# Kernel optimization log

Measured on AMD Instinct MI355X. Metric: run time of the kernel, lower is better.

## Reference

```python
import jax, jax.numpy as jnp
import numpy as np

B, N, S, H = 8, 512, 4096, 1024

def setup_inputs() -> dict:
    key = jax.random.key(0)
    k1, k2, k3 = jax.random.split(key, 3)
    doc_state = jax.random.normal(k1, (B, S, H), dtype=jnp.float32)
    # token->node membership mask (soft weights in [0,1), structurally a sparse/binary mask)
    nodes_mapping = jax.random.uniform(k2, (B, N, S), dtype=jnp.float32)
    # node lengths: positive, in [1, S) to avoid divide-by-near-zero
    nodes_len = jax.random.uniform(k3, (B, N), dtype=jnp.float32, minval=1.0, maxval=float(S))
    return {"doc_state": doc_state, "nodes_mapping": nodes_mapping, "nodes_len": nodes_len}

def reference(doc_state, nodes_mapping, nodes_len):
    # Faithful math: sum_s nodes_mapping[b,n,s] * doc_state[b,s,h] / nodes_len[b,n]
    # Expressed as a batched matmul instead of materializing [B,N,S,H].
    pooled = jnp.einsum('bns,bsh->bnh', nodes_mapping, doc_state)
    return pooled / nodes_len[:, :, None]
```

## Files before the change

kernel.cpp:

```cpp
#include <hip/hip_runtime.h>
#include <hip/hip_bf16.h>


typedef __bf16 bf16x8 __attribute__((ext_vector_type(8)));
typedef float  f32x4  __attribute__((ext_vector_type(4)));

#define MFMA16(a, b, c) __builtin_amdgcn_mfma_f32_16x16x32_bf16(a, b, c, 0, 0, 0)

constexpr int Bsz = 8;
constexpr int Nn  = 512;
constexpr int Ss  = 4096;
constexpr int Hh  = 1024;

constexpr int BM = 64, BN = 64, BK = 32;
constexpr int LDK = BK + 8;
constexpr int NT = Ss / BK;
constexpr int NWG = Bsz * (Nn / BM) * (Hh / BN);

__global__ __launch_bounds__(256, 4)
void mean_pool_gemm(const float* __restrict__ doc,
                    const float* __restrict__ map,
                    const float* __restrict__ len,
                    float* __restrict__ out)
{
    __shared__ __align__(16) __bf16 As[2][BM * LDK];
    __shared__ __align__(16) __bf16 Bs[2][BN * LDK];

    const int blk = (blockIdx.x & 7) * (NWG / 8) + (blockIdx.x >> 3);

    const int b   = blk >> 7;
    const int rem = blk & 127;
    const int mt  = rem >> 4;
    const int ht  = rem & 15;
    const int n0  = mt * BM;
    const int h0  = ht * BN;

    const int tid  = threadIdx.x;
    const int wave = tid >> 6;
    const int lane = tid & 63;
    const int wr   = wave >> 1;
    const int wc   = wave & 1;
    const int l15  = lane & 15;
    const int l4   = lane >> 4;

    const float* Ab = map + (size_t)b * Nn * Ss + (size_t)n0 * Ss;
    const float* Bb = doc + (size_t)b * Ss * Hh + h0;

    const int ra = tid >> 2;
    const int ka = (tid & 3) * 8;
    const int hbb = tid & 63;
    const int kb  = tid >> 6;

    f32x4 aR[2];
    float bR[8];
    f32x4 acc[2][2] = {};

    {
        const float* ap = Ab + (size_t)ra * Ss + ka;
        aR[0] = *(const f32x4*)(ap);
        aR[1] = *(const f32x4*)(ap + 4);
        const float* bp = Bb + (size_t)(kb * 8) * Hh + hbb;
        #pragma unroll
        for (int j = 0; j < 8; j++) bR[j] = bp[(size_t)j * Hh];

        bf16x8 va, vb;
        #pragma unroll
        for (int i = 0; i < 8; i++) {
            va[i] = (__bf16)aR[i >> 2][i & 3];
            vb[i] = (__bf16)bR[i];
        }
        *(bf16x8*)&As[0][ra * LDK + ka]      = va;
        *(bf16x8*)&Bs[0][hbb * LDK + kb * 8] = vb;
    }
    __syncthreads();

    int cur = 0;
    for (int t = 0; t < NT; ++t) {
        if (t + 1 < NT) {
            const int s0 = (t + 1) * BK;
            const float* ap = Ab + (size_t)ra * Ss + s0 + ka;
            aR[0] = *(const f32x4*)(ap);
            aR[1] = *(const f32x4*)(ap + 4);
            const float* bp = Bb + (size_t)(s0 + kb * 8) * Hh + hbb;
            #pragma unroll
            for (int j = 0; j < 8; j++) bR[j] = bp[(size_t)j * Hh];
        }

        {
            bf16x8 aF[2], bF[2];
            #pragma unroll
            for (int m = 0; m < 2; m++)
                aF[m] = *(const bf16x8*)&As[cur][(wr * 32 + m * 16 + l15) * LDK + l4 * 8];
            #pragma unroll
            for (int n = 0; n < 2; n++)
                bF[n] = *(const bf16x8*)&Bs[cur][(wc * 32 + n * 16 + l15) * LDK + l4 * 8];
            #pragma unroll
            for (int m = 0; m < 2; m++)
                #pragma unroll
                for (int n = 0; n < 2; n++)
                    acc[m][n] = MFMA16(aF[m], bF[n], acc[m][n]);
        }

        if (t + 1 < NT) {
            __syncthreads();
            bf16x8 va, vb;
            #pragma unroll
            for (int i = 0; i < 8; i++) {
                va[i] = (__bf16)aR[i >> 2][i & 3];
                vb[i] = (__bf16)bR[i];
            }
            *(bf16x8*)&As[cur ^ 1][ra * LDK + ka]      = va;
            *(bf16x8*)&Bs[cur ^ 1][hbb * LDK + kb * 8] = vb;
            __syncthreads();
            cur ^= 1;
        }
    }

    const float* lenb = len + b * Nn + n0 + wr * 32;
    float* ob = out + (size_t)b * Nn * Hh + (size_t)(n0 + wr * 32) * Hh + h0 + wc * 32;
    #pragma unroll
    for (int m = 0; m < 2; m++) {
        float inv[4];
        #pragma unroll
        for (int j = 0; j < 4; j++) inv[j] = 1.0f / lenb[m * 16 + l4 * 4 + j];
        #pragma unroll
        for (int n = 0; n < 2; n++) {
            #pragma unroll
            for (int j = 0; j < 4; j++) {
                const int row = m * 16 + l4 * 4 + j;
                ob[(size_t)row * Hh + n * 16 + l15] = acc[m][n][j] * inv[j];
            }
        }
    }
}

extern "C" void kernel_launch(void* const* d_in, const int* in_sizes, int n_in,
                              void* d_out, int out_size, void* d_ws, size_t ws_size,
                              hipStream_t stream) {
    const float* doc = (const float*)d_in[0];
    const float* map = (const float*)d_in[1];
    const float* len = (const float*)d_in[2];
    float* out = (float*)d_out;

    dim3 grid(NWG);
    dim3 block(256);
    hipLaunchKernelGGL(mean_pool_gemm, grid, block, 0, stream, doc, map, len, out);
}
```

Baseline: 316.9 us.

## Enlarge M tile and pipeline loads with one barrier per K step

Doubles the M tile to 128 rows, so each workgroup computes a 4x2 grid of MFMA fragments per wave. This halves how many workgroups re-read each doc_state tile. The K loop is unrolled by two, with two register stage sets and two LDS buffers. Each step issues global loads two tiles ahead, converts and stores the previous stage to LDS, computes on the current buffer, and then hits a single barrier instead of two. The cost is more registers, with launch bounds dropping to 2 blocks per CU, and a grid of only 512 workgroups.

```diff
diff --git a/kernel.cpp b/kernel.cpp
--- a/kernel.cpp
+++ b/kernel.cpp
@@ -12,24 +12,68 @@
 constexpr int Ss  = 4096;
 constexpr int Hh  = 1024;
 
-constexpr int BM = 64, BN = 64, BK = 32;
-constexpr int LDK = BK + 8;
-constexpr int NT = Ss / BK;
+constexpr int BM = 128, BN = 64, BK = 32;
+constexpr int LDK = 40;
+constexpr int NT  = Ss / BK;
 constexpr int NWG = Bsz * (Nn / BM) * (Hh / BN);
 
-__global__ __launch_bounds__(256, 4)
+struct StageRegs {
+    f32x4 a[4];
+    float b[8];
+};
+
+__device__ __forceinline__ void issue_loads(StageRegs& r, const float* Ab, const float* Bb,
+                                            int s0, int ra, int ka, int hbb, int kb) {
+    const float* ap = Ab + (size_t)ra * Ss + s0 + ka;
+    #pragma unroll
+    for (int i = 0; i < 4; i++) r.a[i] = *(const f32x4*)(ap + i * 4);
+    const float* bp = Bb + (size_t)(s0 + kb * 8) * Hh + hbb;
+    #pragma unroll
+    for (int j = 0; j < 8; j++) r.b[j] = bp[(size_t)j * Hh];
+}
+
+__device__ __forceinline__ void write_lds(__bf16* As, __bf16* Bs, const StageRegs& r,
+                                          int ra, int ka, int hbb, int kb) {
+    bf16x8 v0, v1, w;
+    #pragma unroll
+    for (int i = 0; i < 8; i++) {
+        v0[i] = (__bf16)r.a[i >> 2][i & 3];
+        v1[i] = (__bf16)r.a[2 + (i >> 2)][i & 3];
+        w[i]  = (__bf16)r.b[i];
+    }
+    *(bf16x8*)&As[ra * LDK + ka]     = v0;
+    *(bf16x8*)&As[ra * LDK + ka + 8] = v1;
+    *(bf16x8*)&Bs[hbb * LDK + kb * 8] = w;
+}
+
+__device__ __forceinline__ void compute(const __bf16* As, const __bf16* Bs,
+                                        f32x4 acc[4][2], int wr, int wc, int l15, int l4) {
+    bf16x8 aF[4], bF[2];
+    #pragma unroll
+    for (int m = 0; m < 4; m++)
+        aF[m] = *(const bf16x8*)&As[(wr * 64 + m * 16 + l15) * LDK + l4 * 8];
+    #pragma unroll
+    for (int n = 0; n < 2; n++)
+        bF[n] = *(const bf16x8*)&Bs[(wc * 32 + n * 16 + l15) * LDK + l4 * 8];
+    #pragma unroll
+    for (int m = 0; m < 4; m++)
+        #pragma unroll
+        for (int n = 0; n < 2; n++)
+            acc[m][n] = MFMA16(aF[m], bF[n], acc[m][n]);
+}
+
+__global__ __launch_bounds__(256, 2)
 void mean_pool_gemm(const float* __restrict__ doc,
                     const float* __restrict__ map,
                     const float* __restrict__ len,
                     float* __restrict__ out)
 {
-    __shared__ __align__(16) __bf16 As[2][BM * LDK];
-    __shared__ __align__(16) __bf16 Bs[2][BN * LDK];
+    __shared__ __align__(16) __bf16 As0[BM * LDK], As1[BM * LDK];
+    __shared__ __align__(16) __bf16 Bs0[BN * LDK], Bs1[BN * LDK];
 
     const int blk = (blockIdx.x & 7) * (NWG / 8) + (blockIdx.x >> 3);
-
-    const int b   = blk >> 7;
-    const int rem = blk & 127;
+    const int b   = blk >> 6;
+    const int rem = blk & 63;
     const int mt  = rem >> 4;
     const int ht  = rem & 15;
     const int n0  = mt * BM;
@@ -46,80 +90,43 @@
     const float* Ab = map + (size_t)b * Nn * Ss + (size_t)n0 * Ss;
     const float* Bb = doc + (size_t)b * Ss * Hh + h0;
 
-    const int ra = tid >> 2;
-    const int ka = (tid & 3) * 8;
+    const int ra = tid >> 1;
+    const int ka = (tid & 1) * 16;
     const int hbb = tid & 63;
     const int kb  = tid >> 6;
 
-    f32x4 aR[2];
-    float bR[8];
-    f32x4 acc[2][2] = {};
+    StageRegs r0, r1;
+    f32x4 acc[4][2] = {};
 
-    {
-        const float* ap = Ab + (size_t)ra * Ss + ka;
-        aR[0] = *(const f32x4*)(ap);
-        aR[1] = *(const f32x4*)(ap + 4);
-        const float* bp = Bb + (size_t)(kb * 8) * Hh + hbb;
-        #pragma unroll
-        for (int j = 0; j < 8; j++) bR[j] = bp[(size_t)j * Hh];
+    issue_loads(r0, Ab, Bb, 0,  ra, ka, hbb, kb);
+    issue_loads(r1, Ab, Bb, BK, ra, ka, hbb, kb);
+    write_lds(As0, Bs0, r0, ra, ka, hbb, kb);
+    asm volatile("s_waitcnt lgkmcnt(0)" ::: "memory");
+    __builtin_amdgcn_s_barrier();
 
-        bf16x8 va, vb;
-        #pragma unroll
-        for (int i = 0; i < 8; i++) {
-            va[i] = (__bf16)aR[i >> 2][i & 3];
-            vb[i] = (__bf16)bR[i];
+    for (int t = 0; t < NT; t += 2) {
+        {
+            const int s2 = (t + 2 < NT ? t + 2 : NT - 1) * BK;
+            issue_loads(r0, Ab, Bb, s2, ra, ka, hbb, kb);
+            write_lds(As1, Bs1, r1, ra, ka, hbb, kb);
+            compute(As0, Bs0, acc, wr, wc, l15, l4);
+            asm volatile("s_waitcnt lgkmcnt(0)" ::: "memory");
+            __builtin_amdgcn_s_barrier();
         }
-        *(bf16x8*)&As[0][ra * LDK + ka]      = va;
-        *(bf16x8*)&Bs[0][hbb * LDK + kb * 8] = vb;
-    }
-    __syncthreads();
-
-    int cur = 0;
-    for (int t = 0; t < NT; ++t) {
-        if (t + 1 < NT) {
-            const int s0 = (t + 1) * BK;
-            const float* ap = Ab + (size_t)ra * Ss + s0 + ka;
-            aR[0] = *(const f32x4*)(ap);
-            aR[1] = *(const f32x4*)(ap + 4);
-            const float* bp = Bb + (size_t)(s0 + kb * 8) * Hh + hbb;
-            #pragma unroll
-            for (int j = 0; j < 8; j++) bR[j] = bp[(size_t)j * Hh];
-        }
-
         {
-            bf16x8 aF[2], bF[2];
-            #pragma unroll
-            for (int m = 0; m < 2; m++)
-                aF[m] = *(const bf16x8*)&As[cur][(wr * 32 + m * 16 + l15) * LDK + l4 * 8];
-            #pragma unroll
-            for (int n = 0; n < 2; n++)
-                bF[n] = *(const bf16x8*)&Bs[cur][(wc * 32 + n * 16 + l15) * LDK + l4 * 8];
-            #pragma unroll
-            for (int m = 0; m < 2; m++)
-                #pragma unroll
-                for (int n = 0; n < 2; n++)
-                    acc[m][n] = MFMA16(aF[m], bF[n], acc[m][n]);
-        }
-
-        if (t + 1 < NT) {
-            __syncthreads();
-            bf16x8 va, vb;
-            #pragma unroll
-            for (int i = 0; i < 8; i++) {
-                va[i] = (__bf16)aR[i >> 2][i & 3];
-                vb[i] = (__bf16)bR[i];
-            }
-            *(bf16x8*)&As[cur ^ 1][ra * LDK + ka]      = va;
-            *(bf16x8*)&Bs[cur ^ 1][hbb * LDK + kb * 8] = vb;
-            __syncthreads();
-            cur ^= 1;
+            const int s3 = (t + 3 < NT ? t + 3 : NT - 1) * BK;
+            issue_loads(r1, Ab, Bb, s3, ra, ka, hbb, kb);
+            write_lds(As0, Bs0, r0, ra, ka, hbb, kb);
+            compute(As1, Bs1, acc, wr, wc, l15, l4);
+            asm volatile("s_waitcnt lgkmcnt(0)" ::: "memory");
+            __builtin_amdgcn_s_barrier();
         }
     }
 
-    const float* lenb = len + b * Nn + n0 + wr * 32;
-    float* ob = out + (size_t)b * Nn * Hh + (size_t)(n0 + wr * 32) * Hh + h0 + wc * 32;
+    const float* lenb = len + b * Nn + n0 + wr * 64;
+    float* ob = out + (size_t)b * Nn * Hh + (size_t)(n0 + wr * 64) * Hh + h0 + wc * 32;
     #pragma unroll
-    for (int m = 0; m < 2; m++) {
+    for (int m = 0; m < 4; m++) {
         float inv[4];
         #pragma unroll
         for (int j = 0; j < 4; j++) inv[j] = 1.0f / lenb[m * 16 + l4 * 4 + j];
```

New measurement: 342.7 us. +8.1%, slower.
